# Kernel tuning notes

Hardware: AMD Instinct MI355X
Metric: run time of the kernel (lower is better)

## Reference

```python
import jax, jax.numpy as jnp
import numpy as np

SQRT2 = 1.4142135623730951  # fused_leaky_relu gain
DN = ('NCHW', 'OIHW', 'NCHW')


def _setup_filter():
    # upfirdn2d.setup_filter([1,3,3,1]): separable outer product, normalized to sum 1
    f = jnp.array([1., 3., 3., 1.], dtype=jnp.float32)
    f = f / jnp.sum(f)
    return jnp.outer(f, f)  # [4,4], symmetric so flip is a no-op


def _depthwise_fir(x, f2, pad, down):
    # upfirdn2d: depthwise conv with the 4x4 resample filter
    C = x.shape[1]
    k = jnp.broadcast_to(f2[None, None], (C, 1, 4, 4)).astype(x.dtype)
    return jax.lax.conv_general_dilated(
        x, k, window_strides=(down, down),
        padding=[(pad, pad), (pad, pad)],
        feature_group_count=C, dimension_numbers=DN)


def _conv(x, w, stride, pad):
    return jax.lax.conv_general_dilated(
        x, w, window_strides=(stride, stride),
        padding=[(pad, pad), (pad, pad)], dimension_numbers=DN)


def _act(x):
    # fused_leaky_relu with no bias: leaky_relu(x, 0.2) * sqrt(2)
    return jax.nn.leaky_relu(x, negative_slope=0.2) * SQRT2


def setup_inputs() -> dict:
    key = jax.random.key(0)
    k1, k2, k3, k4 = jax.random.split(key, 4)
    N, Cin, Cout, H = 16, 256, 512, 64
    return {
        'latents_in': jax.random.normal(k1, (N, Cin, H, H), dtype=jnp.float32),
        'w_conv': jax.random.normal(k2, (Cin, Cin, 3, 3), dtype=jnp.float32),
        'w_down': jax.random.normal(k3, (Cout, Cin, 3, 3), dtype=jnp.float32),
        'w_skip': jax.random.normal(k4, (Cout, Cin, 1, 1), dtype=jnp.float32),
    }


def reference(latents_in, w_conv, w_down, w_skip):
    f2 = _setup_filter()
    Cin = w_conv.shape[1]
    g3 = 1.0 / np.sqrt(Cin * 9)   # weight_gain for 3x3 convs
    g1 = 1.0 / np.sqrt(Cin)       # weight_gain for 1x1 skip conv

    y = latents_in
    # self.conv: 3x3, pad 1, stride 1, no bias, fused leaky relu
    x = _act(_conv(y, w_conv * g3, stride=1, pad=1))
    # self.conv_down: FIR lowpass (pad 2) then 3x3 conv stride 2 (conv2d_resample down=2)
    x = _depthwise_fir(x, f2, pad=2, down=1)          # [N,Cin,H+1,H+1]
    out = _act(_conv(x, w_down * g3, stride=2, pad=0))  # [N,Cout,H/2,H/2]
    # skip path: downsample2d(y) then 1x1 conv (no bias) + act
    skip = _depthwise_fir(y, f2, pad=1, down=2)       # [N,Cin,H/2,H/2]
    skip = _act(_conv(skip, w_skip * g1, stride=1, pad=0))
    return skip + out
```

## Files before the change

kernel.cpp:

```cpp
#include <hip/hip_runtime.h>
#include <hip/hip_bf16.h>
#include <stdint.h>


typedef __bf16 bf8v __attribute__((ext_vector_type(8)));
typedef float  f4   __attribute__((ext_vector_type(4)));

#define G3F (1.0f / 48.0f)
#define G1F (1.0f / 16.0f)
#define SQRT2F 1.4142135623730951f

__device__ __forceinline__ float actf(float v) {
    return (v > 0.0f ? v : 0.2f * v) * SQRT2F;
}
__device__ __forceinline__ unsigned short f2bu(float f) {
    __hip_bfloat16 h = __float2bfloat16(f);
    return *reinterpret_cast<unsigned short*>(&h);
}
__device__ __forceinline__ bf8v ld8(const __hip_bfloat16* p) {
    return *reinterpret_cast<const bf8v*>(p);
}
__device__ __forceinline__ void llds16(const __hip_bfloat16* g, void* l) {
    __builtin_amdgcn_global_load_lds(
        (const __attribute__((address_space(1))) unsigned int*)g,
        (__attribute__((address_space(3))) unsigned int*)l, 16, 0, 0);
}

__global__ __launch_bounds__(256) void p_misc(__hip_bfloat16* __restrict__ xb,
                                              __hip_bfloat16* __restrict__ zbuf,
                                              const float* __restrict__ wconv,
                                              __hip_bfloat16* __restrict__ wA,
                                              const float* __restrict__ wdown,
                                              __hip_bfloat16* __restrict__ wD,
                                              const float* __restrict__ wskip,
                                              __hip_bfloat16* __restrict__ wst) {
    int b = blockIdx.x, t = threadIdx.x;
    if (b < 256) {
        int idx = b * 256 + t;
        int c8 = idx & 31, side = (idx >> 5) & 1, h = (idx >> 6) & 63, n = idx >> 12;
        int wp = side * 65;
        uint4 z = {0, 0, 0, 0};
        *reinterpret_cast<uint4*>(xb + (((size_t)(n * 64 + h) * 66 + wp) << 8) + c8 * 8) = z;
        if (b == 0 && t < 64)
            *reinterpret_cast<uint4*>(zbuf + (t << 3)) = z;
    } else if (b < 544) {
        int idx = (b - 256) * 256 + t;
        int lane = idx & 63;
        int co16 = (idx >> 6) & 15;
        int q    = (idx >> 10) & 7;
        int tp   = idx >> 13;
        int co = co16 * 16 + (lane & 15);
        int ci = q * 32 + (lane >> 4) * 8;
        union { uint4 v; unsigned short h8[8]; } pk;
        #pragma unroll
        for (int e = 0; e < 8; ++e)
            pk.h8[e] = f2bu(wconv[(size_t)(co * 256 + ci + e) * 9 + tp] * G3F);
        *reinterpret_cast<uint4*>(wA + (size_t)idx * 8) = pk.v;
    } else if (b < 1120) {
        int idx = (b - 544) * 256 + t;
        int lane = idx & 63;
        int co16 = (idx >> 6) & 31;
        int q    = (idx >> 11) & 7;
        int tp   = idx >> 14;
        int co = co16 * 16 + (lane & 15);
        int ci = q * 32 + (lane >> 4) * 8;
        union { uint4 v; unsigned short h8[8]; } pk;
        #pragma unroll
        for (int e = 0; e < 8; ++e)
            pk.h8[e] = f2bu(wdown[(size_t)(co * 256 + ci + e) * 9 + tp] * G3F);
        *reinterpret_cast<uint4*>(wD + (size_t)idx * 8) = pk.v;
    } else {
        int idx = (b - 1120) * 256 + t;
        wst[idx] = __float2bfloat16(wskip[idx] * G1F);
    }
}

__global__ __launch_bounds__(256) void p_xb(const float* __restrict__ lat,
                                            __hip_bfloat16* __restrict__ xb) {
    __shared__ float tile[32][65];
    int bx = blockIdx.x;
    int cic = bx & 7, h = (bx >> 3) & 63, n = bx >> 9;
    int ci0 = cic * 32;
    int t = threadIdx.x;
    {
        int cir = t >> 3, wq = (t & 7) * 8;
        const float* src = lat + (((size_t)(n * 256 + ci0 + cir) * 64 + h) * 64 + wq);
        float4 v0 = *(const float4*)src;
        float4 v1 = *(const float4*)(src + 4);
        tile[cir][wq + 0] = v0.x; tile[cir][wq + 1] = v0.y;
        tile[cir][wq + 2] = v0.z; tile[cir][wq + 3] = v0.w;
        tile[cir][wq + 4] = v1.x; tile[cir][wq + 5] = v1.y;
        tile[cir][wq + 6] = v1.z; tile[cir][wq + 7] = v1.w;
    }
    __syncthreads();
    {
        int w = t >> 2, c8 = (t & 3) * 8;
        union { uint4 q; unsigned short h8[8]; } pk;
        #pragma unroll
        for (int j = 0; j < 8; ++j) pk.h8[j] = f2bu(tile[c8 + j][w]);
        __hip_bfloat16* dst = xb + (((size_t)(n * 64 + h) * 66 + (w + 1)) << 8) + ci0 + c8;
        *reinterpret_cast<uint4*>(dst) = pk.q;
    }
}

__global__ __launch_bounds__(256) void k_fir2n(const __hip_bfloat16* __restrict__ xb,
                                               __hip_bfloat16* __restrict__ s2) {
    int idx = blockIdx.x * 256 + threadIdx.x;
    int c8 = idx & 31, ow = (idx >> 5) & 31, oh = (idx >> 10) & 31, n = idx >> 15;
    const float fk[4] = {0.125f, 0.375f, 0.375f, 0.125f};
    float a8[8];
    #pragma unroll
    for (int e = 0; e < 8; ++e) a8[e] = 0.0f;
    const __hip_bfloat16* src = xb + ((size_t)n * 64 * 66) * 256 + c8 * 8;
    #pragma unroll
    for (int i = 0; i < 4; ++i) {
        int rr = 2 * oh + i - 1;
        if ((unsigned)rr >= 64u) continue;
        #pragma unroll
        for (int j = 0; j < 4; ++j) {
            int wp = 2 * ow + j;
            bf8v v = ld8(src + ((size_t)(rr * 66 + wp) << 8));
            float fw = fk[i] * fk[j];
            #pragma unroll
            for (int e = 0; e < 8; ++e) a8[e] += fw * (float)v[e];
        }
    }
    union { uint4 q; unsigned short h8[8]; } pk;
    #pragma unroll
    for (int e = 0; e < 8; ++e) pk.h8[e] = f2bu(a8[e]);
    *reinterpret_cast<uint4*>(s2 + (((size_t)(n * 1024 + oh * 32 + ow)) << 8) + c8 * 8) = pk.q;
}

__global__ __launch_bounds__(256) void k_skipg(const __hip_bfloat16* __restrict__ s2,
                                               const __hip_bfloat16* __restrict__ wst,
                                               float* __restrict__ out) {
    const int lane = threadIdx.x & 63;
    const int wid  = threadIdx.x >> 6;
    const int wr = wid & 1, wc = wid >> 1;
    const int l15 = lane & 15, g = lane >> 4;

    int raw = blockIdx.x;
    int lg  = (raw & 7) * 64 + (raw >> 3);
    int cot = lg >> 7, pxt = lg & 127;
    int n = pxt >> 3, oh0 = (pxt & 7) * 4;

    f4 acc[4][4];
    #pragma unroll
    for (int m = 0; m < 4; ++m)
        #pragma unroll
        for (int nf = 0; nf < 4; ++nf)
            #pragma unroll
            for (int e = 0; e < 4; ++e) acc[m][nf][e] = 0.0f;

    #pragma unroll
    for (int k = 0; k < 8; ++k) {
        bf8v a_[4], b_[4];
        #pragma unroll
        for (int nf = 0; nf < 4; ++nf) {
            int oh = oh0 + wc * 2 + (nf >> 1);
            int ow = (nf & 1) * 16 + l15;
            b_[nf] = ld8(s2 + (((size_t)(n * 1024 + oh * 32 + ow)) << 8) + k * 32 + g * 8);
        }
        #pragma unroll
        for (int m = 0; m < 4; ++m) {
            int co = cot * 128 + wr * 64 + m * 16 + l15;
            a_[m] = ld8(wst + (size_t)co * 256 + k * 32 + g * 8);
        }
        #pragma unroll
        for (int m = 0; m < 4; ++m)
            #pragma unroll
            for (int nf = 0; nf < 4; ++nf)
                acc[m][nf] = __builtin_amdgcn_mfma_f32_16x16x32_bf16(
                    a_[m], b_[nf], acc[m][nf], 0, 0, 0);
    }
    #pragma unroll
    for (int m = 0; m < 4; ++m)
        #pragma unroll
        for (int nf = 0; nf < 4; ++nf) {
            f4 v = acc[m][nf];
            int oh = oh0 + wc * 2 + (nf >> 1);
            int ow = (nf & 1) * 16 + l15;
            int co = cot * 128 + wr * 64 + m * 16 + 4 * g;
            #pragma unroll
            for (int r = 0; r < 4; ++r)
                out[((size_t)(n * 512 + co + r)) * 1024 + oh * 32 + ow] = actf(v[r]);
        }
}

__global__ __launch_bounds__(256, 4) void k_conv1s(const __hip_bfloat16* __restrict__ xb,
                                                   const __hip_bfloat16* __restrict__ wA,
                                                   const __hip_bfloat16* __restrict__ zbuf,
                                                   __hip_bfloat16* __restrict__ x1) {
    __shared__ uint4 smq[2112];
    char* smc = (char*)smq;
    const int tid  = threadIdx.x;
    const int lane = tid & 63;
    const int wid  = tid >> 6;
    const int wr = wid & 1, wc = wid >> 1;
    const int l15 = lane & 15, g = lane >> 4;

    int raw = blockIdx.x;
    int lg  = (raw & 7) * 128 + (raw >> 3);
    int cot = lg >> 9, pxt = lg & 511;
    int n = pxt >> 5, h0 = (pxt & 31) * 2;
    const size_t nb66 = (size_t)n * 64 * 66 * 256;
    const size_t nb   = (size_t)n * 4096 * 256;
    const char* wAc = (const char*)wA;

    f4 acc[4][4];
    #pragma unroll
    for (int m = 0; m < 4; ++m)
        #pragma unroll
        for (int nf = 0; nf < 4; ++nf)
            #pragma unroll
            for (int e = 0; e < 4; ++e) acc[m][nf][e] = 0.0f;

    #pragma unroll 1
    for (int ch = 0; ch < 4; ++ch) {
        if (ch) __syncthreads();
        for (int li = wid; li < 33; li += 4) {
            int gi = li * 64 + lane;
            int row = (gi >= 1584) ? 3 : (gi >= 1056) ? 2 : (gi >= 528) ? 1 : 0;
            int rem = gi - row * 528;
            int wp = rem >> 3;
            int c8 = (rem & 7) ^ (wp & 7);
            int rc = h0 - 1 + row;
            const __hip_bfloat16* src = ((unsigned)rc < 64u)
                ? xb + nb66 + (((size_t)(rc * 66 + wp)) << 8) + ch * 64 + c8 * 8
                : zbuf + (lane << 3);
            llds16(src, smc + li * 1024);
        }
        __syncthreads();

        auto loadBf = [&](int p, int nf) -> bf8v {
            int tap = p >> 1, qq = p & 1;
            int kh = tap / 3, kw = tap % 3;
            int wp = nf * 16 + l15 + kw;
            int c8r = qq * 4 + g;
            int off = (wc + kh) * 8448 + (wp * 8 + (c8r ^ (wp & 7))) * 16;
            return *(const bf8v*)(smc + off);
        };
        auto loadAf = [&](int p, int m) -> bf8v {
            int tap = p >> 1, q = ch * 2 + (p & 1);
            return *(const bf8v*)(wAc +
                ((size_t)((tap * 8 + q) * 16 + cot * 8 + wr * 4 + m) << 10) +
                (lane << 4));
        };

        bf8v aF[4], bF[4];
        #pragma unroll
        for (int nf = 0; nf < 4; ++nf) bF[nf] = loadBf(0, nf);
        #pragma unroll
        for (int m = 0; m < 4; ++m) aF[m] = loadAf(0, m);

        #pragma unroll
        for (int p = 0; p < 18; ++p) {
            const bool lastp = (p == 17);
            #pragma unroll
            for (int m = 0; m < 3; ++m) {
                #pragma unroll
                for (int nf = 0; nf < 4; ++nf)
                    acc[m][nf] = __builtin_amdgcn_mfma_f32_16x16x32_bf16(
                        aF[m], bF[nf], acc[m][nf], 0, 0, 0);
                if (!lastp) aF[m] = loadAf(p + 1, m);
            }
            #pragma unroll
            for (int nf = 0; nf < 4; ++nf) {
                acc[3][nf] = __builtin_amdgcn_mfma_f32_16x16x32_bf16(
                    aF[3], bF[nf], acc[3][nf], 0, 0, 0);
                if (!lastp) bF[nf] = loadBf(p + 1, nf);
            }
            if (!lastp) aF[3] = loadAf(p + 1, 3);
        }
    }

    __syncthreads();
    #pragma unroll
    for (int m = 0; m < 4; ++m)
        #pragma unroll
        for (int nf = 0; nf < 4; ++nf) {
            int p = wc * 64 + nf * 16 + l15;
            int co4 = wr * 16 + m * 4 + g;
            int co4s = co4 ^ ((p & 15) << 1);
            union { unsigned long long u; unsigned short h4[4]; } pk;
            #pragma unroll
            for (int r = 0; r < 4; ++r) pk.h4[r] = f2bu(actf(acc[m][nf][r]));
            *reinterpret_cast<unsigned long long*>(smc + p * 256 + co4s * 8) = pk.u;
        }
    __syncthreads();
    {
        int p = tid >> 1, coh = tid & 1;
        int hh = h0 + (p >> 6), w = p & 63;
        __hip_bfloat16* dst = x1 + nb + (((size_t)(hh * 64 + w)) << 8) + cot * 128 + coh * 64;
        #pragma unroll
        for (int j = 0; j < 8; ++j) {
            int r2 = coh * 8 + j;
            int co4s = (2 * r2) ^ ((p & 15) << 1);
            uint4 v = *reinterpret_cast<const uint4*>(smc + p * 256 + co4s * 8);
            *reinterpret_cast<uint4*>(dst + j * 8) = v;
        }
    }
}

__global__ __launch_bounds__(256) void k_fir1(const __hip_bfloat16* __restrict__ x1,
                                              __hip_bfloat16* __restrict__ xf) {
    int idx = blockIdx.x * 256 + threadIdx.x;
    int c8 = idx & 31; int rest = idx >> 5;
    int owq = rest % 17; rest /= 17;
    int oh = rest % 65; int n = rest / 65;
    int ow0 = owq * 4; if (ow0 > 61) ow0 = 61;
    int ci = c8 * 8;
    const float fk[4] = {0.125f, 0.375f, 0.375f, 0.125f};
    const __hip_bfloat16* src = x1 + (size_t)n * 4096 * 256 + ci;

    float t[7][8];
    #pragma unroll
    for (int c = 0; c < 7; ++c) {
        #pragma unroll
        for (int e = 0; e < 8; ++e) t[c][e] = 0.0f;
        int col = ow0 - 2 + c;
        if ((unsigned)col >= 64u) continue;
        #pragma unroll
        for (int i = 0; i < 4; ++i) {
            int r = oh + i - 2;
            if ((unsigned)r >= 64u) continue;
            bf8v v = ld8(src + ((size_t)(r * 64 + col) << 8));
            float fw = fk[i];
            #pragma unroll
            for (int e = 0; e < 8; ++e) t[c][e] += fw * (float)v[e];
        }
    }
    #pragma unroll
    for (int o = 0; o < 4; ++o) {
        union { uint4 q; unsigned short h8[8]; } pk;
        #pragma unroll
        for (int e = 0; e < 8; ++e) {
            float s = fk[0] * t[o][e] + fk[1] * t[o + 1][e] +
                      fk[2] * t[o + 2][e] + fk[3] * t[o + 3][e];
            pk.h8[e] = f2bu(s);
        }
        *reinterpret_cast<uint4*>(
            xf + ((size_t)n * 4225 + oh * 65 + ow0 + o) * 256 + ci) = pk.q;
    }
}

__global__ __launch_bounds__(256, 4) void k_downs(const __hip_bfloat16* __restrict__ xf,
                                                  const __hip_bfloat16* __restrict__ wD,
                                                  float* __restrict__ out) {
    __shared__ uint4 smq[1344];
    char* smc = (char*)smq;
    const int tid  = threadIdx.x;
    const int lane = tid & 63;
    const int wid  = tid >> 6;
    const int l15  = lane & 15, g = lane >> 4;

    int raw = blockIdx.x;
    int lg  = (raw & 7) * 128 + (raw >> 3);
    int cot = lg >> 8;
    int rest = lg & 255;
    int n = rest >> 4, oht = rest & 15;
    int r0 = oht * 4;
    const size_t nxf = (size_t)n * 4225 * 256;
    const char* wDc = (const char*)wD;

    f4 acc[2][4];
    #pragma unroll
    for (int m = 0; m < 2; ++m)
        #pragma unroll
        for (int nf = 0; nf < 4; ++nf)
            #pragma unroll
            for (int e = 0; e < 4; ++e) acc[m][nf][e] = 0.0f;

    #pragma unroll 1
    for (int ch = 0; ch < 8; ++ch) {
        if (ch) __syncthreads();
        for (int li = wid; li < 21; li += 4) {
            int gi = li * 64 + lane;
            if (gi > 1319) gi = 1319;
            int row = (gi >= 1056) ? 4 : (gi >= 792) ? 3 : (gi >= 528) ? 2 :
                      (gi >= 264) ? 1 : 0;
            int rem = gi - row * 264;
            int wpair = rem >> 3;
            int t4 = (rem & 7) ^ (wpair & 7);
            int odd = t4 >> 2, c8 = t4 & 3;
            int wp = wpair * 2 + odd; if (wp > 64) wp = 64;
            const __hip_bfloat16* src = xf + nxf +
                (((size_t)((r0 + row) * 65 + wp)) << 8) + ch * 32 + c8 * 8;
            llds16(src, smc + li * 1024);
        }
        __syncthreads();

        auto loadBf = [&](int p, int nf) -> bf8v {
            int kh = p / 3, kw = p % 3;
            int ow = (nf & 1) * 16 + l15;
            int wp = 2 * ow + kw;
            int wpair = wp >> 1, odd = wp & 1;
            int s8 = (g + 4 * odd) ^ (wpair & 7);
            int off = ((2 * (nf >> 1) + kh) * 264 + wpair * 8 + s8) * 16;
            return *(const bf8v*)(smc + off);
        };
        auto loadAf = [&](int p, int m) -> bf8v {
            return *(const bf8v*)(wDc +
                ((size_t)((p * 8 + ch) * 32 + cot * 8 + wid * 2 + m) << 10) +
                (lane << 4));
        };

        bf8v aF[2], bF[4];
        #pragma unroll
        for (int nf = 0; nf < 4; ++nf) bF[nf] = loadBf(0, nf);
        #pragma unroll
        for (int m = 0; m < 2; ++m) aF[m] = loadAf(0, m);

        #pragma unroll
        for (int p = 0; p < 9; ++p) {
            const bool lastp = (p == 8);
            #pragma unroll
            for (int nf = 0; nf < 4; ++nf)
                acc[0][nf] = __builtin_amdgcn_mfma_f32_16x16x32_bf16(
                    aF[0], bF[nf], acc[0][nf], 0, 0, 0);
            if (!lastp) aF[0] = loadAf(p + 1, 0);
            #pragma unroll
            for (int nf = 0; nf < 4; ++nf) {
                acc[1][nf] = __builtin_amdgcn_mfma_f32_16x16x32_bf16(
                    aF[1], bF[nf], acc[1][nf], 0, 0, 0);
                if (!lastp) bF[nf] = loadBf(p + 1, nf);
            }
            if (!lastp) aF[1] = loadAf(p + 1, 1);
        }
    }

    #pragma unroll
    for (int m = 0; m < 2; ++m)
        #pragma unroll
        for (int nf = 0; nf < 4; ++nf) {
            f4 v = acc[m][nf];
            int oh = oht * 2 + (nf >> 1);
            int ow = (nf & 1) * 16 + l15;
            int co = cot * 128 + wid * 32 + m * 16 + 4 * g;
            #pragma unroll
            for (int r = 0; r < 4; ++r) {
                size_t oi = ((size_t)(n * 512 + co + r)) * 1024 + oh * 32 + ow;
                out[oi] += actf(v[r]);
            }
        }
}

extern "C" void kernel_launch(void* const* d_in, const int* in_sizes, int n_in,
                              void* d_out, int out_size, void* d_ws, size_t ws_size,
                              hipStream_t stream) {
    const float* lat   = (const float*)d_in[0];
    const float* wconv = (const float*)d_in[1];
    const float* wdown = (const float*)d_in[2];
    const float* wskip = (const float*)d_in[3];
    float* out = (float*)d_out;

    char* base = (char*)d_ws;
    __hip_bfloat16* xb   = (__hip_bfloat16*)base;
    __hip_bfloat16* xf   = (__hip_bfloat16*)base;
    __hip_bfloat16* x1   = (__hip_bfloat16*)(base + 34611200);
    __hip_bfloat16* s2   = (__hip_bfloat16*)(base + 34611200);
    __hip_bfloat16* wA   = (__hip_bfloat16*)(base + 68165632);
    __hip_bfloat16* wD   = (__hip_bfloat16*)(base + 69345280);
    __hip_bfloat16* wst  = (__hip_bfloat16*)(base + 71704576);
    __hip_bfloat16* zbuf = (__hip_bfloat16*)(base + 71966720);

    hipLaunchKernelGGL(p_misc, dim3(1632), dim3(256), 0, stream,
                       xb, zbuf, wconv, wA, wdown, wD, wskip, wst);
    hipLaunchKernelGGL(p_xb,    dim3(8192), dim3(256), 0, stream, lat,   xb);
    hipLaunchKernelGGL(k_fir2n, dim3(2048), dim3(256), 0, stream, xb, s2);
    hipLaunchKernelGGL(k_skipg, dim3(512),  dim3(256), 0, stream, s2, wst, out);
    hipLaunchKernelGGL(k_conv1s, dim3(1024), dim3(256), 0, stream, xb, wA, zbuf, x1);
    hipLaunchKernelGGL(k_fir1,  dim3(2210), dim3(256), 0, stream, x1, xf);
    hipLaunchKernelGGL(k_downs, dim3(1024), dim3(256), 0, stream, xf, wD, out);
}
```

Measured before the change: 241.1 us.

## Double-buffer LDS staging in conv kernels and remap block-to-tile ordering

Converts the 3x3 conv and strided down-conv kernels from single-buffered LDS staging to double-buffered staging. The next channel chunk is prefetched asynchronously while MFMAs run on the current one. k_conv1s moves to smaller 32-channel chunks with a new swizzle, and all three kernels now interleave output-channel tiles innermost so blocks sharing input pixels run close together. The cost is more LDS per block and a lower occupancy hint for k_downs. The explicit register prefetch of A/B fragments is dropped.

Result: slower. 263.1 us (+9.1%).

```diff
diff --git a/kernel.cpp b/kernel.cpp
--- a/kernel.cpp
+++ b/kernel.cpp
@@ -141,7 +141,7 @@
 
     int raw = blockIdx.x;
     int lg  = (raw & 7) * 64 + (raw >> 3);
-    int cot = lg >> 7, pxt = lg & 127;
+    int cot = lg & 3, pxt = lg >> 2;
     int n = pxt >> 3, oh0 = (pxt & 7) * 4;
 
     f4 acc[4][4];
@@ -191,7 +191,7 @@
                                                    const __hip_bfloat16* __restrict__ wA,
                                                    const __hip_bfloat16* __restrict__ zbuf,
                                                    __hip_bfloat16* __restrict__ x1) {
-    __shared__ uint4 smq[2112];
+    __shared__ uint4 smq[2176];
     char* smc = (char*)smq;
     const int tid  = threadIdx.x;
     const int lane = tid & 63;
@@ -201,7 +201,7 @@
 
     int raw = blockIdx.x;
     int lg  = (raw & 7) * 128 + (raw >> 3);
-    int cot = lg >> 9, pxt = lg & 511;
+    int cot = lg & 1, pxt = lg >> 1;
     int n = pxt >> 5, h0 = (pxt & 31) * 2;
     const size_t nb66 = (size_t)n * 64 * 66 * 256;
     const size_t nb   = (size_t)n * 4096 * 256;
@@ -215,66 +215,58 @@
             #pragma unroll
             for (int e = 0; e < 4; ++e) acc[m][nf][e] = 0.0f;
 
-    #pragma unroll 1
-    for (int ch = 0; ch < 4; ++ch) {
-        if (ch) __syncthreads();
-        for (int li = wid; li < 33; li += 4) {
+    auto stage = [&](int ch, char* dst) {
+        #pragma unroll
+        for (int li2 = 0; li2 < 5; ++li2) {
+            int li = wid + 4 * li2;
+            if (li >= 17) break;
             int gi = li * 64 + lane;
-            int row = (gi >= 1584) ? 3 : (gi >= 1056) ? 2 : (gi >= 528) ? 1 : 0;
-            int rem = gi - row * 528;
-            int wp = rem >> 3;
-            int c8 = (rem & 7) ^ (wp & 7);
+            if (gi > 1055) gi = 1055;
+            int row = (gi >= 792) ? 3 : (gi >= 528) ? 2 : (gi >= 264) ? 1 : 0;
+            int rem = gi - row * 264;
+            int wp = rem >> 2;
+            int c8 = (rem & 3) ^ (wp & 3);
             int rc = h0 - 1 + row;
             const __hip_bfloat16* src = ((unsigned)rc < 64u)
-                ? xb + nb66 + (((size_t)(rc * 66 + wp)) << 8) + ch * 64 + c8 * 8
+                ? xb + nb66 + (((size_t)(rc * 66 + wp)) << 8) + ch * 32 + c8 * 8
                 : zbuf + (lane << 3);
-            llds16(src, smc + li * 1024);
-        }
-        __syncthreads();
-
-        auto loadBf = [&](int p, int nf) -> bf8v {
-            int tap = p >> 1, qq = p & 1;
-            int kh = tap / 3, kw = tap % 3;
-            int wp = nf * 16 + l15 + kw;
-            int c8r = qq * 4 + g;
-            int off = (wc + kh) * 8448 + (wp * 8 + (c8r ^ (wp & 7))) * 16;
-            return *(const bf8v*)(smc + off);
-        };
-        auto loadAf = [&](int p, int m) -> bf8v {
-            int tap = p >> 1, q = ch * 2 + (p & 1);
-            return *(const bf8v*)(wAc +
-                ((size_t)((tap * 8 + q) * 16 + cot * 8 + wr * 4 + m) << 10) +
-                (lane << 4));
-        };
-
-        bf8v aF[4], bF[4];
-        #pragma unroll
-        for (int nf = 0; nf < 4; ++nf) bF[nf] = loadBf(0, nf);
-        #pragma unroll
-        for (int m = 0; m < 4; ++m) aF[m] = loadAf(0, m);
-
-        #pragma unroll
-        for (int p = 0; p < 18; ++p) {
-            const bool lastp = (p == 17);
-            #pragma unroll
-            for (int m = 0; m < 3; ++m) {
+            llds16(src, dst + li * 1024);
+        }
+    };
+
+    stage(0, smc);
+    __syncthreads();
+
+    #pragma unroll 1
+    for (int ch = 0; ch < 8; ++ch) {
+        const char* buf = smc + (ch & 1) * 17408;
+        char* nxt       = smc + ((ch + 1) & 1) * 17408;
+        if (ch < 7) stage(ch + 1, nxt);
+
+        #pragma unroll
+        for (int p = 0; p < 9; ++p) {
+            int kh = p / 3, kw = p % 3;
+            bf8v b_[4];
+            #pragma unroll
+            for (int nf = 0; nf < 4; ++nf) {
+                int wp = nf * 16 + l15 + kw;
+                int off = (wc + kh) * 4224 + (wp << 6) + ((g ^ (wp & 3)) << 4);
+                b_[nf] = *(const bf8v*)(buf + off);
+            }
+            #pragma unroll
+            for (int m = 0; m < 4; ++m) {
+                bf8v a = *(const bf8v*)(wAc +
+                    ((size_t)((p * 8 + ch) * 16 + cot * 8 + wr * 4 + m) << 10) +
+                    (lane << 4));
                 #pragma unroll
                 for (int nf = 0; nf < 4; ++nf)
                     acc[m][nf] = __builtin_amdgcn_mfma_f32_16x16x32_bf16(
-                        aF[m], bF[nf], acc[m][nf], 0, 0, 0);
-                if (!lastp) aF[m] = loadAf(p + 1, m);
+                        a, b_[nf], acc[m][nf], 0, 0, 0);
             }
-            #pragma unroll
-            for (int nf = 0; nf < 4; ++nf) {
-                acc[3][nf] = __builtin_amdgcn_mfma_f32_16x16x32_bf16(
-                    aF[3], bF[nf], acc[3][nf], 0, 0, 0);
-                if (!lastp) bF[nf] = loadBf(p + 1, nf);
-            }
-            if (!lastp) aF[3] = loadAf(p + 1, 3);
-        }
-    }
-
-    __syncthreads();
+        }
+        __syncthreads();
+    }
+
     #pragma unroll
     for (int m = 0; m < 4; ++m)
         #pragma unroll
@@ -344,10 +336,10 @@
     }
 }
 
-__global__ __launch_bounds__(256, 4) void k_downs(const __hip_bfloat16* __restrict__ xf,
+__global__ __launch_bounds__(256, 3) void k_downs(const __hip_bfloat16* __restrict__ xf,
                                                   const __hip_bfloat16* __restrict__ wD,
                                                   float* __restrict__ out) {
-    __shared__ uint4 smq[1344];
+    __shared__ uint4 smq[2688];
     char* smc = (char*)smq;
     const int tid  = threadIdx.x;
     const int lane = tid & 63;
@@ -356,8 +348,8 @@
 
     int raw = blockIdx.x;
     int lg  = (raw & 7) * 128 + (raw >> 3);
-    int cot = lg >> 8;
-    int rest = lg & 255;
+    int cot = lg & 3;
+    int rest = lg >> 2;
     int n = rest >> 4, oht = rest & 15;
     int r0 = oht * 4;
     const size_t nxf = (size_t)n * 4225 * 256;
@@ -371,10 +363,11 @@
             #pragma unroll
             for (int e = 0; e < 4; ++e) acc[m][nf][e] = 0.0f;
 
-    #pragma unroll 1
-    for (int ch = 0; ch < 8; ++ch) {
-        if (ch) __syncthreads();
-        for (int li = wid; li < 21; li += 4) {
+    auto stage = [&](int ch, char* dst) {
+        #pragma unroll
+        for (int li2 = 0; li2 < 6; ++li2) {
+            int li = wid + 4 * li2;
+            if (li >= 21) break;
             int gi = li * 64 + lane;
             if (gi > 1319) gi = 1319;
             int row = (gi >= 1056) ? 4 : (gi >= 792) ? 3 : (gi >= 528) ? 2 :
@@ -386,47 +379,44 @@
             int wp = wpair * 2 + odd; if (wp > 64) wp = 64;
             const __hip_bfloat16* src = xf + nxf +
                 (((size_t)((r0 + row) * 65 + wp)) << 8) + ch * 32 + c8 * 8;
-            llds16(src, smc + li * 1024);
+            llds16(src, dst + li * 1024);
+        }
+    };
+
+    stage(0, smc);
+    __syncthreads();
+
+    #pragma unroll 1
+    for (int ch = 0; ch < 8; ++ch) {
+        const char* buf = smc + (ch & 1) * 21504;
+        char* nxt       = smc + ((ch + 1) & 1) * 21504;
+        if (ch < 7) stage(ch + 1, nxt);
+
+        #pragma unroll
+        for (int p = 0; p < 9; ++p) {
+            int kh = p / 3, kw = p % 3;
+            bf8v b_[4];
+            #pragma unroll
+            for (int nf = 0; nf < 4; ++nf) {
+                int ow = (nf & 1) * 16 + l15;
+                int wp = 2 * ow + kw;
+                int wpair = wp >> 1, odd = wp & 1;
+                int s8 = (g + 4 * odd) ^ (wpair & 7);
+                int off = ((2 * (nf >> 1) + kh) * 264 + wpair * 8 + s8) * 16;
+                b_[nf] = *(const bf8v*)(buf + off);
+            }
+            #pragma unroll
+            for (int m = 0; m < 2; ++m) {
+                bf8v a = *(const bf8v*)(wDc +
+                    ((size_t)((p * 8 + ch) * 32 + cot * 8 + wid * 2 + m) << 10) +
+                    (lane << 4));
+                #pragma unroll
+                for (int nf = 0; nf < 4; ++nf)
+                    acc[m][nf] = __builtin_amdgcn_mfma_f32_16x16x32_bf16(
+                        a, b_[nf], acc[m][nf], 0, 0, 0);
+            }
         }
         __syncthreads();
-
-        auto loadBf = [&](int p, int nf) -> bf8v {
-            int kh = p / 3, kw = p % 3;
-            int ow = (nf & 1) * 16 + l15;
-            int wp = 2 * ow + kw;
-            int wpair = wp >> 1, odd = wp & 1;
-            int s8 = (g + 4 * odd) ^ (wpair & 7);
-            int off = ((2 * (nf >> 1) + kh) * 264 + wpair * 8 + s8) * 16;
-            return *(const bf8v*)(smc + off);
-        };
-        auto loadAf = [&](int p, int m) -> bf8v {
-            return *(const bf8v*)(wDc +
-                ((size_t)((p * 8 + ch) * 32 + cot * 8 + wid * 2 + m) << 10) +
-                (lane << 4));
-        };
-
-        bf8v aF[2], bF[4];
-        #pragma unroll
-        for (int nf = 0; nf < 4; ++nf) bF[nf] = loadBf(0, nf);
-        #pragma unroll
-        for (int m = 0; m < 2; ++m) aF[m] = loadAf(0, m);
-
-        #pragma unroll
-        for (int p = 0; p < 9; ++p) {
-            const bool lastp = (p == 8);
-            #pragma unroll
-            for (int nf = 0; nf < 4; ++nf)
-                acc[0][nf] = __builtin_amdgcn_mfma_f32_16x16x32_bf16(
-                    aF[0], bF[nf], acc[0][nf], 0, 0, 0);
-            if (!lastp) aF[0] = loadAf(p + 1, 0);
-            #pragma unroll
-            for (int nf = 0; nf < 4; ++nf) {
-                acc[1][nf] = __builtin_amdgcn_mfma_f32_16x16x32_bf16(
-                    aF[1], bF[nf], acc[1][nf], 0, 0, 0);
-                if (!lastp) bF[nf] = loadBf(p + 1, nf);
-            }
-            if (!lastp) aF[1] = loadAf(p + 1, 1);
-        }
     }
 
     #pragma unroll
```

## Double-buffer LDS staging in k_downs and reorder block-to-tile mapping

Applied to the files above, without the earlier changes.

The downsampling conv kernel now double-buffers its LDS input tile, issuing the async global-to-LDS load for the next channel chunk while MFMAs run on the current one. The LDS allocation doubles and the launch bound drops from 4 to 3 blocks per SM. The register prefetch of A and B fragments is replaced by a plain load-then-MFMA sequence. In both k_skipg and k_downs the output-channel tile becomes the fastest-varying index, so blocks sharing the same input pixels run close together and can reuse them in cache. The cost is lower occupancy and less software prefetching inside each chunk.

Measured after the change: 231.1 us. -4.2%, faster.

```diff
diff --git a/kernel.cpp b/kernel.cpp
--- a/kernel.cpp
+++ b/kernel.cpp
@@ -141,7 +141,7 @@
 
     int raw = blockIdx.x;
     int lg  = (raw & 7) * 64 + (raw >> 3);
-    int cot = lg >> 7, pxt = lg & 127;
+    int cot = lg & 3, pxt = lg >> 2;
     int n = pxt >> 3, oh0 = (pxt & 7) * 4;
 
     f4 acc[4][4];
@@ -344,10 +344,10 @@
     }
 }
 
-__global__ __launch_bounds__(256, 4) void k_downs(const __hip_bfloat16* __restrict__ xf,
+__global__ __launch_bounds__(256, 3) void k_downs(const __hip_bfloat16* __restrict__ xf,
                                                   const __hip_bfloat16* __restrict__ wD,
                                                   float* __restrict__ out) {
-    __shared__ uint4 smq[1344];
+    __shared__ uint4 smq[2688];
     char* smc = (char*)smq;
     const int tid  = threadIdx.x;
     const int lane = tid & 63;
@@ -356,8 +356,8 @@
 
     int raw = blockIdx.x;
     int lg  = (raw & 7) * 128 + (raw >> 3);
-    int cot = lg >> 8;
-    int rest = lg & 255;
+    int cot = lg & 3;
+    int rest = lg >> 2;
     int n = rest >> 4, oht = rest & 15;
     int r0 = oht * 4;
     const size_t nxf = (size_t)n * 4225 * 256;
@@ -371,10 +371,11 @@
             #pragma unroll
             for (int e = 0; e < 4; ++e) acc[m][nf][e] = 0.0f;
 
-    #pragma unroll 1
-    for (int ch = 0; ch < 8; ++ch) {
-        if (ch) __syncthreads();
-        for (int li = wid; li < 21; li += 4) {
+    auto stage = [&](int ch, char* dst) {
+        #pragma unroll
+        for (int li2 = 0; li2 < 6; ++li2) {
+            int li = wid + 4 * li2;
+            if (li >= 21) break;
             int gi = li * 64 + lane;
             if (gi > 1319) gi = 1319;
             int row = (gi >= 1056) ? 4 : (gi >= 792) ? 3 : (gi >= 528) ? 2 :
@@ -386,47 +387,44 @@
             int wp = wpair * 2 + odd; if (wp > 64) wp = 64;
             const __hip_bfloat16* src = xf + nxf +
                 (((size_t)((r0 + row) * 65 + wp)) << 8) + ch * 32 + c8 * 8;
-            llds16(src, smc + li * 1024);
+            llds16(src, dst + li * 1024);
+        }
+    };
+
+    stage(0, smc);
+    __syncthreads();
+
+    #pragma unroll 1
+    for (int ch = 0; ch < 8; ++ch) {
+        const char* buf = smc + (ch & 1) * 21504;
+        char* nxt       = smc + ((ch + 1) & 1) * 21504;
+        if (ch < 7) stage(ch + 1, nxt);
+
+        #pragma unroll
+        for (int p = 0; p < 9; ++p) {
+            int kh = p / 3, kw = p % 3;
+            bf8v b_[4];
+            #pragma unroll
+            for (int nf = 0; nf < 4; ++nf) {
+                int ow = (nf & 1) * 16 + l15;
+                int wp = 2 * ow + kw;
+                int wpair = wp >> 1, odd = wp & 1;
+                int s8 = (g + 4 * odd) ^ (wpair & 7);
+                int off = ((2 * (nf >> 1) + kh) * 264 + wpair * 8 + s8) * 16;
+                b_[nf] = *(const bf8v*)(buf + off);
+            }
+            #pragma unroll
+            for (int m = 0; m < 2; ++m) {
+                bf8v a = *(const bf8v*)(wDc +
+                    ((size_t)((p * 8 + ch) * 32 + cot * 8 + wid * 2 + m) << 10) +
+                    (lane << 4));
+                #pragma unroll
+                for (int nf = 0; nf < 4; ++nf)
+                    acc[m][nf] = __builtin_amdgcn_mfma_f32_16x16x32_bf16(
+                        a, b_[nf], acc[m][nf], 0, 0, 0);
+            }
         }
         __syncthreads();
-
-        auto loadBf = [&](int p, int nf) -> bf8v {
-            int kh = p / 3, kw = p % 3;
-            int ow = (nf & 1) * 16 + l15;
-            int wp = 2 * ow + kw;
-            int wpair = wp >> 1, odd = wp & 1;
-            int s8 = (g + 4 * odd) ^ (wpair & 7);
-            int off = ((2 * (nf >> 1) + kh) * 264 + wpair * 8 + s8) * 16;
-            return *(const bf8v*)(smc + off);
-        };
-        auto loadAf = [&](int p, int m) -> bf8v {
-            return *(const bf8v*)(wDc +
-                ((size_t)((p * 8 + ch) * 32 + cot * 8 + wid * 2 + m) << 10) +
-                (lane << 4));
-        };
-
-        bf8v aF[2], bF[4];
-        #pragma unroll
-        for (int nf = 0; nf < 4; ++nf) bF[nf] = loadBf(0, nf);
-        #pragma unroll
-        for (int m = 0; m < 2; ++m) aF[m] = loadAf(0, m);
-
-        #pragma unroll
-        for (int p = 0; p < 9; ++p) {
-            const bool lastp = (p == 8);
-            #pragma unroll
-            for (int nf = 0; nf < 4; ++nf)
-                acc[0][nf] = __builtin_amdgcn_mfma_f32_16x16x32_bf16(
-                    aF[0], bF[nf], acc[0][nf], 0, 0, 0);
-            if (!lastp) aF[0] = loadAf(p + 1, 0);
-            #pragma unroll
-            for (int nf = 0; nf < 4; ++nf) {
-                acc[1][nf] = __builtin_amdgcn_mfma_f32_16x16x32_bf16(
-                    aF[1], bF[nf], acc[1][nf], 0, 0, 0);
-                if (!lastp) bF[nf] = loadBf(p + 1, nf);
-            }
-            if (!lastp) aF[1] = loadAf(p + 1, 1);
-        }
     }
 
     #pragma unroll
```
